# Kernel optimization log

Measured on AMD Instinct MI355X. Metric: run time of the kernel, lower is better.

## Reference

```python
import jax, jax.numpy as jnp
import numpy as np
from jax import lax

V, E, H = 32000, 512, 1024  # vocab, embedding_dim, hidden_dim
S, B, T = 50, 64, 10        # src len, batch, max decode steps
SOS = 0


def setup_inputs() -> dict:
    key = jax.random.key(0)
    ks = jax.random.split(key, 16)
    sc = 0.02
    n = jax.random.normal
    return {
        "enc_out": n(ks[0], (S, B, 2 * H), jnp.float32),
        "hidden": n(ks[1], (1, B, H), jnp.float32),
        "target": jax.random.randint(ks[2], (B, T), 0, V),
        "emb": n(ks[3], (V, E), jnp.float32) * sc,
        "w_ih": n(ks[4], (3 * H, E), jnp.float32) * sc,
        "w_hh": n(ks[5], (3 * H, H), jnp.float32) * sc,
        "b_ih": n(ks[6], (3 * H,), jnp.float32) * sc,
        "b_hh": n(ks[7], (3 * H,), jnp.float32) * sc,
        "wa_w": n(ks[8], (H, H), jnp.float32) * sc,
        "wa_b": n(ks[9], (H,), jnp.float32) * sc,
        "ua_w": n(ks[10], (H, 2 * H), jnp.float32) * sc,
        "ua_b": n(ks[11], (H,), jnp.float32) * sc,
        "va_w": n(ks[12], (1, H), jnp.float32) * sc,
        "va_b": n(ks[13], (1,), jnp.float32) * sc,
    }


def reference(enc_out, hidden, target, emb, w_ih, w_hh, b_ih, b_hh,
              wa_w, wa_b, ua_w, ua_b, va_w, va_b):
    b, t = target.shape

    def gru_cell(x, h):
        gi = x @ w_ih.T + b_ih          # [B, 3H]
        gh = h @ w_hh.T + b_hh          # [B, 3H]
        ir, iz, inn = jnp.split(gi, 3, axis=-1)
        hr, hz, hn = jnp.split(gh, 3, axis=-1)
        r = jax.nn.sigmoid(ir + hr)
        z = jax.nn.sigmoid(iz + hz)
        nng = jnp.tanh(inn + r * hn)
        return (1.0 - z) * nng + z * h

    # teacher-forced decoder inputs: [SOS, target[:, :-1]] -> [T, B]
    dec_in = jnp.concatenate(
        [jnp.full((b, 1), SOS, dtype=target.dtype), target[:, : t - 1]], axis=1)
    xs = emb[dec_in].transpose(1, 0, 2)  # [T, B, E] (dropout is identity in eval)

    def step(h, x):
        h2 = gru_cell(x, h)
        return h2, h2

    h_last, hs = lax.scan(step, hidden[0], xs)   # hs: [T, B, H]

    keys = enc_out.transpose(1, 0, 2)            # [B, S, 2H]
    uk = keys @ ua_w.T + ua_b                    # [B, S, H]
    wq = hs @ wa_w.T + wa_b                      # [T, B, H]
    # additive (Bahdanau) scores: [T, B, S]
    scores = (jnp.tanh(wq[:, :, None, :] + uk[None]) @ va_w.T + va_b)[..., 0]
    weights = jax.nn.softmax(scores, axis=-1)    # over source positions
    context = jnp.einsum('tbs,bsd->btd', weights, keys)  # [B, T, 2H]
    out = jax.nn.log_softmax(context, axis=-1)   # [B, T, 2H]
    return out, h_last
```

## Files before the change

kernel.cpp:

```cpp
#include <hip/hip_runtime.h>
#include <math.h>

#define VOCAB 32000
#define E_DIM 512
#define H_DIM 1024
#define S_LEN 50
#define B_SZ 64
#define T_LEN 10
#define H3 (3 * H_DIM)
#define D2H (2 * H_DIM)

typedef __attribute__((ext_vector_type(8))) short short8;
typedef __attribute__((ext_vector_type(4))) float floatx4;

__device__ __forceinline__ ushort f2b(float f) {
    union { float f; uint32_t u; } x; x.f = f;
    uint32_t r = (x.u + 0x7fff + ((x.u >> 16) & 1)) >> 16;
    return (ushort)r;
}
__device__ __forceinline__ float b2f(ushort u) {
    union { float f; uint32_t u; } x; x.u = ((uint32_t)u) << 16;
    return x.f;
}
__device__ __forceinline__ float fast_sigmoid(float x) {
    x = fminf(fmaxf(x, -30.f), 30.f);
    return 1.f / (1.f + __expf(-x));
}
__device__ __forceinline__ float fast_tanh(float x) {
    x = fminf(fmaxf(x, -15.f), 15.f);
    float e = __expf(2.f * x);
    return (e - 1.f) / (e + 1.f);
}

#define PB0 1536
#define PB1 (PB0 + 3072)
#define PB2 (PB1 + 2048)
#define PB3 (PB2 + 1024)
#define PB4 (PB3 + 3200)
#define PB5 (PB4 + 640)
#define PB6 (PB5 + 64)

__device__ __forceinline__ void cvt_chunk(const float* src, ushort* dst, int i) {
    float4 v = ((const float4*)src)[i];
    ushort4 o;
    o.x = f2b(v.x); o.y = f2b(v.y); o.z = f2b(v.z); o.w = f2b(v.w);
    ((ushort4*)dst)[i] = o;
}

__global__ __launch_bounds__(256) void prep(
    const float* __restrict__ w_ih, ushort* __restrict__ w_ihb,
    const float* __restrict__ w_hh, ushort* __restrict__ w_hhb,
    const float* __restrict__ ua_w, ushort* __restrict__ ua_wb,
    const float* __restrict__ wa_w, ushort* __restrict__ wa_wb,
    const float* __restrict__ enc_out, ushort* __restrict__ keysb,
    const int* __restrict__ target, const float* __restrict__ emb,
    ushort* __restrict__ Xb,
    const float* __restrict__ hidden, ushort* __restrict__ hb0,
    int* __restrict__ bar) {
    int bid = blockIdx.x, tid = threadIdx.x;
    if (bid == 0 && tid < 8) bar[tid] = 0;
    if (bid < PB0) {
        cvt_chunk(w_ih, w_ihb, bid * 256 + tid);
    } else if (bid < PB1) {
        cvt_chunk(w_hh, w_hhb, (bid - PB0) * 256 + tid);
    } else if (bid < PB2) {
        cvt_chunk(ua_w, ua_wb, (bid - PB1) * 256 + tid);
    } else if (bid < PB3) {
        cvt_chunk(wa_w, wa_wb, (bid - PB2) * 256 + tid);
    } else if (bid < PB4) {
        int bs = bid - PB3;
        int b = bs / S_LEN, s = bs % S_LEN;
        const float* src = enc_out + ((size_t)s * B_SZ + b) * D2H;
        ushort* dst = keysb + (size_t)bs * D2H;
#pragma unroll
        for (int p = 0; p < 2; ++p) {
            int i = tid + p * 256;
            float4 v = ((const float4*)src)[i];
            ushort4 o;
            o.x = f2b(v.x); o.y = f2b(v.y); o.z = f2b(v.z); o.w = f2b(v.w);
            ((ushort4*)dst)[i] = o;
        }
    } else if (bid < PB5) {
        int m = bid - PB4;
        int t = m / B_SZ, b = m % B_SZ;
        int idx = (t == 0) ? 0 : target[b * T_LEN + (t - 1)];
        if (tid < 128) {
            const float* src = emb + (size_t)idx * E_DIM;
            float4 v = ((const float4*)src)[tid];
            ushort4 o;
            o.x = f2b(v.x); o.y = f2b(v.y); o.z = f2b(v.z); o.w = f2b(v.w);
            ((ushort4*)(Xb + (size_t)m * E_DIM))[tid] = o;
        }
    } else {
        cvt_chunk(hidden, hb0, (bid - PB5) * 256 + tid);
    }
}

struct GemmArgs {
    const ushort* A; const ushort* W; const float* bias;
    float* Cf; ushort* C16;
    int M, N, K, nbn, nblk;
};

__global__ __launch_bounds__(256) void gemm_bf16(GemmArgs g0, GemmArgs g1) {
    const bool first = (int)blockIdx.x < g0.nblk;
    GemmArgs g = first ? g0 : g1;
    const int bid = first ? blockIdx.x : (blockIdx.x - g0.nblk);

    __shared__ ushort As[64 * 72];
    __shared__ ushort Bs[128 * 72];

    const int tid = threadIdx.x;
    const int w = tid >> 6, lane = tid & 63;
    const int lm = lane & 15, q = lane >> 4;
    const int wm = w >> 1, wn = w & 1;
    const int n0 = (bid % g.nbn) * 128;
    const int m0 = (bid / g.nbn) * 64;
    const int K = g.K;

    floatx4 acc[2][4];
#pragma unroll
    for (int i = 0; i < 2; ++i)
#pragma unroll
        for (int j = 0; j < 4; ++j)
            acc[i][j] = (floatx4){0.f, 0.f, 0.f, 0.f};

    short8 ar[2], br[4];
    auto load_tiles = [&](int k0) {
#pragma unroll
        for (int p = 0; p < 2; ++p) {
            int c = tid + p * 256;
            ar[p] = *(const short8*)&g.A[(size_t)(m0 + (c >> 3)) * K + k0 + (c & 7) * 8];
        }
#pragma unroll
        for (int p = 0; p < 4; ++p) {
            int c = tid + p * 256;
            br[p] = *(const short8*)&g.W[(size_t)(n0 + (c >> 3)) * K + k0 + (c & 7) * 8];
        }
    };

    load_tiles(0);
    for (int k0 = 0; k0 < K; k0 += 64) {
#pragma unroll
        for (int p = 0; p < 2; ++p) {
            int c = tid + p * 256;
            *(short8*)&As[(c >> 3) * 72 + (c & 7) * 8] = ar[p];
        }
#pragma unroll
        for (int p = 0; p < 4; ++p) {
            int c = tid + p * 256;
            *(short8*)&Bs[(c >> 3) * 72 + (c & 7) * 8] = br[p];
        }
        __syncthreads();
        if (k0 + 64 < K) load_tiles(k0 + 64);

#pragma unroll
        for (int kk = 0; kk < 2; ++kk) {
            short8 af[2], bf[4];
#pragma unroll
            for (int i = 0; i < 2; ++i)
                af[i] = *(const short8*)&As[(wm * 32 + i * 16 + lm) * 72 + kk * 32 + q * 8];
#pragma unroll
            for (int j = 0; j < 4; ++j)
                bf[j] = *(const short8*)&Bs[(wn * 64 + j * 16 + lm) * 72 + kk * 32 + q * 8];
#pragma unroll
            for (int i = 0; i < 2; ++i)
#pragma unroll
                for (int j = 0; j < 4; ++j)
                    acc[i][j] = __builtin_amdgcn_mfma_f32_16x16x32_bf16(af[i], bf[j], acc[i][j], 0, 0, 0);
        }
        __syncthreads();
    }

    float bv[4];
#pragma unroll
    for (int j = 0; j < 4; ++j)
        bv[j] = g.bias[n0 + wn * 64 + j * 16 + lm];
#pragma unroll
    for (int i = 0; i < 2; ++i) {
#pragma unroll
        for (int j = 0; j < 4; ++j) {
            int col = n0 + wn * 64 + j * 16 + lm;
#pragma unroll
            for (int r = 0; r < 4; ++r) {
                int row = m0 + wm * 32 + i * 16 + q * 4 + r;
                float v = acc[i][j][r] + bv[j];
                if (g.C16) g.C16[(size_t)row * g.N + col] = f2b(v);
                else       g.Cf[(size_t)row * g.N + col] = v;
            }
        }
    }
}

#define GRU_BLOCKS 64

__device__ __forceinline__ void grid_barrier(int* cnt, int* gen, int phase) {
    __syncthreads();
    if (threadIdx.x == 0) {
        __threadfence();
        if (atomicAdd(cnt, 1) == GRU_BLOCKS - 1) {
            atomicExch(cnt, 0);
            __threadfence();
            atomicExch(gen, phase + 1);
        } else {
            while (atomicAdd(gen, 0) <= phase) __builtin_amdgcn_s_sleep(8);
        }
        __threadfence();
    }
    __syncthreads();
}

__global__ __launch_bounds__(256) void gru_persistent(
    const ushort* __restrict__ w_hhb, const float* __restrict__ bhh,
    const float* __restrict__ GI, const float* __restrict__ hidden,
    ushort* __restrict__ hb0, ushort* __restrict__ hb1,
    ushort* __restrict__ hsb, float* __restrict__ outTail,
    int* __restrict__ bar) {
    __shared__ ushort Ws[2][48 * 136];
    const int tid = threadIdx.x;
    const int w = tid >> 6, lane = tid & 63;
    const int lm = lane & 15, q = lane >> 4;
    const int j0 = blockIdx.x * 16;
    const int j = j0 + lm;

    const float bhr = bhh[j], bhz = bhh[H_DIM + j], bhn = bhh[2 * H_DIM + j];

    float hf[4];
#pragma unroll
    for (int r = 0; r < 4; ++r)
        hf[r] = hidden[(size_t)(w * 16 + q * 4 + r) * H_DIM + j];

    short8 wr[3];
    auto stage_regs = [&](int kbase) {
#pragma unroll
        for (int p = 0; p < 3; ++p) {
            int c = tid + p * 256;
            int row = c >> 4, off = c & 15;
            int grow = (row >> 4) * H_DIM + j0 + (row & 15);
            wr[p] = *(const short8*)&w_hhb[(size_t)grow * H_DIM + kbase + off * 8];
        }
    };
    auto write_lds = [&](int buf) {
#pragma unroll
        for (int p = 0; p < 3; ++p) {
            int c = tid + p * 256;
            *(short8*)&Ws[buf][(c >> 4) * 136 + (c & 15) * 8] = wr[p];
        }
    };

    for (int t = 0; t < T_LEN; ++t) {
        const ushort* hin = (t & 1) ? hb1 : hb0;
        ushort* hout = (t & 1) ? hb0 : hb1;

        float ir[4], iz[4], inn[4];
#pragma unroll
        for (int r = 0; r < 4; ++r) {
            const float* gi = GI + (size_t)(t * B_SZ + w * 16 + q * 4 + r) * H3 + j;
            ir[r] = gi[0]; iz[r] = gi[H_DIM]; inn[r] = gi[2 * H_DIM];
        }

        floatx4 accr = {0.f, 0.f, 0.f, 0.f};
        floatx4 accz = {0.f, 0.f, 0.f, 0.f};
        floatx4 accn = {0.f, 0.f, 0.f, 0.f};

        stage_regs(0);
        write_lds(0);
        const ushort* arow = hin + (size_t)(w * 16 + lm) * H_DIM + q * 8;

        for (int it = 0; it < 8; ++it) {
            __syncthreads();
            if (it < 7) stage_regs((it + 1) * 128);
            short8 af[4];
#pragma unroll
            for (int kk = 0; kk < 4; ++kk)
                af[kk] = *(const short8*)&arow[it * 128 + kk * 32];
            const int buf = it & 1;
#pragma unroll
            for (int kk = 0; kk < 4; ++kk) {
                short8 b0 = *(const short8*)&Ws[buf][(lm) * 136 + kk * 32 + q * 8];
                short8 b1 = *(const short8*)&Ws[buf][(16 + lm) * 136 + kk * 32 + q * 8];
                short8 b2 = *(const short8*)&Ws[buf][(32 + lm) * 136 + kk * 32 + q * 8];
                accr = __builtin_amdgcn_mfma_f32_16x16x32_bf16(af[kk], b0, accr, 0, 0, 0);
                accz = __builtin_amdgcn_mfma_f32_16x16x32_bf16(af[kk], b1, accz, 0, 0, 0);
                accn = __builtin_amdgcn_mfma_f32_16x16x32_bf16(af[kk], b2, accn, 0, 0, 0);
            }
            if (it < 7) write_lds(buf ^ 1);
        }

#pragma unroll
        for (int r = 0; r < 4; ++r) {
            int b = w * 16 + q * 4 + r;
            float rg = fast_sigmoid(ir[r] + accr[r] + bhr);
            float z  = fast_sigmoid(iz[r] + accz[r] + bhz);
            float ng = fast_tanh(inn[r] + rg * (accn[r] + bhn));
            float hnew = (1.f - z) * ng + z * hf[r];
            hf[r] = hnew;
            size_t hi = (size_t)b * H_DIM + j;
            ushort h16 = f2b(hnew);
            hout[hi] = h16;
            hsb[(size_t)t * B_SZ * H_DIM + hi] = h16;
            if (t == T_LEN - 1) outTail[hi] = hnew;
        }

        if (t < T_LEN - 1) grid_barrier(&bar[0], &bar[1], t);
    }
}

__global__ __launch_bounds__(256) void attn_ctx(
    const ushort* __restrict__ WQ16, const ushort* __restrict__ UK16,
    const float* __restrict__ va_w, const float* __restrict__ va_b,
    const ushort* __restrict__ keysb, float* __restrict__ out) {
    __shared__ float wq_s[H_DIM];
    __shared__ float va_s[H_DIM];
    __shared__ float sc[S_LEN];
    __shared__ float wred[4];
    __shared__ float sred[4];
    const int bt = blockIdx.x;
    const int t = bt >> 6, b = bt & 63;
    const int tid = threadIdx.x;
    const int wave = tid >> 6, lane = tid & 63;

    for (int hh = tid; hh < H_DIM; hh += 256) {
        wq_s[hh] = b2f(WQ16[(size_t)(t * B_SZ + b) * H_DIM + hh]);
        va_s[hh] = va_w[hh];
    }
    __syncthreads();

    for (int s = wave; s < S_LEN; s += 4) {
        const ushort* uk = UK16 + ((size_t)b * S_LEN + s) * H_DIM + lane * 16;
        short8 u0 = *(const short8*)&uk[0];
        short8 u1 = *(const short8*)&uk[8];
        float acc = 0.f;
        const int h0 = lane * 16;
#pragma unroll
        for (int i = 0; i < 8; ++i)
            acc += fast_tanh(wq_s[h0 + i] + b2f((ushort)u0[i])) * va_s[h0 + i];
#pragma unroll
        for (int i = 0; i < 8; ++i)
            acc += fast_tanh(wq_s[h0 + 8 + i] + b2f((ushort)u1[i])) * va_s[h0 + 8 + i];
        for (int off = 32; off > 0; off >>= 1) acc += __shfl_down(acc, off);
        if (lane == 0) sc[s] = acc + va_b[0];
    }
    __syncthreads();

    if (tid < 64) {
        float v = (tid < S_LEN) ? sc[tid] : -INFINITY;
        float m = v;
        for (int off = 32; off > 0; off >>= 1) m = fmaxf(m, __shfl_down(m, off));
        m = __shfl(m, 0);
        float e = (tid < S_LEN) ? __expf(v - m) : 0.f;
        float sum = e;
        for (int off = 32; off > 0; off >>= 1) sum += __shfl_down(sum, off);
        sum = __shfl(sum, 0);
        if (tid < S_LEN) sc[tid] = e / sum;
    }
    __syncthreads();

    float c[8];
#pragma unroll
    for (int i = 0; i < 8; ++i) c[i] = 0.f;
    const ushort* kb = keysb + (size_t)b * S_LEN * D2H + tid * 8;
    for (int s = 0; s < S_LEN; ++s) {
        float ws = sc[s];
        short8 kv = *(const short8*)&kb[(size_t)s * D2H];
#pragma unroll
        for (int i = 0; i < 8; ++i) c[i] += ws * b2f((ushort)kv[i]);
    }

    float m = c[0];
#pragma unroll
    for (int i = 1; i < 8; ++i) m = fmaxf(m, c[i]);
    for (int off = 32; off > 0; off >>= 1) m = fmaxf(m, __shfl_down(m, off));
    if (lane == 0) wred[wave] = m;
    __syncthreads();
    if (tid == 0) wred[0] = fmaxf(fmaxf(wred[0], wred[1]), fmaxf(wred[2], wred[3]));
    __syncthreads();
    m = wred[0];
    float sum = 0.f;
#pragma unroll
    for (int i = 0; i < 8; ++i) sum += __expf(c[i] - m);
    for (int off = 32; off > 0; off >>= 1) sum += __shfl_down(sum, off);
    if (lane == 0) sred[wave] = sum;
    __syncthreads();
    if (tid == 0) sred[0] = sred[0] + sred[1] + sred[2] + sred[3];
    __syncthreads();
    float lse = m + __logf(sred[0]);

    float* o = out + ((size_t)b * T_LEN + t) * D2H + tid * 8;
#pragma unroll
    for (int i = 0; i < 8; ++i) o[i] = c[i] - lse;
}

extern "C" void kernel_launch(void* const* d_in, const int* in_sizes, int n_in,
                              void* d_out, int out_size, void* d_ws, size_t ws_size,
                              hipStream_t stream) {
    const float* enc_out = (const float*)d_in[0];
    const float* hidden  = (const float*)d_in[1];
    const int*   target  = (const int*)d_in[2];
    const float* emb     = (const float*)d_in[3];
    const float* w_ih    = (const float*)d_in[4];
    const float* w_hh    = (const float*)d_in[5];
    const float* b_ih    = (const float*)d_in[6];
    const float* b_hh    = (const float*)d_in[7];
    const float* wa_w    = (const float*)d_in[8];
    const float* wa_b    = (const float*)d_in[9];
    const float* ua_w    = (const float*)d_in[10];
    const float* ua_b    = (const float*)d_in[11];
    const float* va_w    = (const float*)d_in[12];
    const float* va_b    = (const float*)d_in[13];
    float* out = (float*)d_out;

    const int TB = T_LEN * B_SZ;
    const int BS = B_SZ * S_LEN;

    char* p = (char*)d_ws;
    int*    bar   = (int*)p;    p += 256;
    float*  GI    = (float*)p;  p += (size_t)TB * H3 * 4;
    p = (char*)(((uintptr_t)p + 255) & ~(uintptr_t)255);
    ushort* keysb = (ushort*)p; p += (size_t)BS * D2H * 2;
    ushort* Xb    = (ushort*)p; p += (size_t)TB * E_DIM * 2;
    ushort* w_ihb = (ushort*)p; p += (size_t)H3 * E_DIM * 2;
    ushort* w_hhb = (ushort*)p; p += (size_t)H3 * H_DIM * 2;
    ushort* ua_wb = (ushort*)p; p += (size_t)H_DIM * D2H * 2;
    ushort* wa_wb = (ushort*)p; p += (size_t)H_DIM * H_DIM * 2;
    ushort* hb0   = (ushort*)p; p += (size_t)B_SZ * H_DIM * 2;
    ushort* hb1   = (ushort*)p; p += (size_t)B_SZ * H_DIM * 2;
    ushort* hsb   = (ushort*)p; p += (size_t)TB * H_DIM * 2;
    ushort* UK16  = (ushort*)p; p += (size_t)BS * H_DIM * 2;
    ushort* WQ16  = (ushort*)p; p += (size_t)TB * H_DIM * 2;

    prep<<<PB6, 256, 0, stream>>>(w_ih, w_ihb, w_hh, w_hhb, ua_w, ua_wb, wa_w, wa_wb,
                                  enc_out, keysb, target, emb, Xb, hidden, hb0, bar);

    GemmArgs guk = { keysb, ua_wb, ua_b, nullptr, UK16,
                     BS, H_DIM, D2H, H_DIM / 128, (BS / 64) * (H_DIM / 128) };
    GemmArgs ggi = { Xb, w_ihb, b_ih, GI, nullptr,
                     TB, H3, E_DIM, H3 / 128, (TB / 64) * (H3 / 128) };
    gemm_bf16<<<guk.nblk + ggi.nblk, 256, 0, stream>>>(guk, ggi);

    float* outTail = out + (size_t)B_SZ * T_LEN * D2H;
    gru_persistent<<<GRU_BLOCKS, 256, 0, stream>>>(w_hhb, b_hh, GI, hidden,
                                                   hb0, hb1, hsb, outTail, bar);

    GemmArgs gwq = { hsb, wa_wb, wa_b, nullptr, WQ16,
                     TB, H_DIM, H_DIM, H_DIM / 128, (TB / 64) * (H_DIM / 128) };
    gemm_bf16<<<gwq.nblk, 256, 0, stream>>>(gwq, gwq);

    attn_ctx<<<B_SZ * T_LEN, 256, 0, stream>>>(WQ16, UK16, va_w, va_b, keysb, out);
}
```

Before: 355.8 us.

## Keep GRU recurrent weight slice resident in LDS and use hierarchical grid barrier

The persistent GRU kernel now loads each block's 48x1024 bf16 slice of w_hh into LDS once, before the time loop, instead of re-streaming it from global memory every step through double-buffered tiles. This removes per-step weight traffic and the per-tile __syncthreads, and the hidden-state A fragments are prefetched one tile ahead. The grid barrier becomes a two-level counter tree with per-step slots (8 groups of 8 blocks, padded to separate lines), using acquire/release atomics and a shorter sleep, to cut contention on a single atomic. The cost is about 99 KB of LDS per block and a larger barrier workspace that prep now zeroes.

```diff
diff --git a/kernel.cpp b/kernel.cpp
--- a/kernel.cpp
+++ b/kernel.cpp
@@ -58,7 +58,9 @@
     const float* __restrict__ hidden, ushort* __restrict__ hb0,
     int* __restrict__ bar) {
     int bid = blockIdx.x, tid = threadIdx.x;
-    if (bid == 0 && tid < 8) bar[tid] = 0;
+    if (bid == 0) {
+        for (int i = tid; i < 4096; i += 256) bar[i] = 0;
+    }
     if (bid < PB0) {
         cvt_chunk(w_ih, w_ihb, bid * 256 + tid);
     } else if (bid < PB1) {
@@ -193,18 +195,25 @@
 }
 
 #define GRU_BLOCKS 64
-
-__device__ __forceinline__ void grid_barrier(int* cnt, int* gen, int phase) {
+#define WS_STRIDE 1032
+
+__device__ __forceinline__ void grid_barrier(int* __restrict__ bar, int t, int bid) {
     __syncthreads();
     if (threadIdx.x == 0) {
         __threadfence();
-        if (atomicAdd(cnt, 1) == GRU_BLOCKS - 1) {
-            atomicExch(cnt, 0);
-            __threadfence();
-            atomicExch(gen, phase + 1);
-        } else {
-            while (atomicAdd(gen, 0) <= phase) __builtin_amdgcn_s_sleep(8);
-        }
+        int g = bid & 7;
+        int sub = __hip_atomic_fetch_add(&bar[(t * 8 + g) * 32], 1,
+                                         __ATOMIC_ACQ_REL, __HIP_MEMORY_SCOPE_AGENT);
+        if (sub == 7) {
+            int m = __hip_atomic_fetch_add(&bar[2560 + t * 32], 1,
+                                           __ATOMIC_ACQ_REL, __HIP_MEMORY_SCOPE_AGENT);
+            if (m == 7)
+                __hip_atomic_store(&bar[3040], t + 1,
+                                   __ATOMIC_RELEASE, __HIP_MEMORY_SCOPE_AGENT);
+        }
+        while (__hip_atomic_load(&bar[3040], __ATOMIC_ACQUIRE,
+                                 __HIP_MEMORY_SCOPE_AGENT) <= t)
+            __builtin_amdgcn_s_sleep(2);
         __threadfence();
     }
     __syncthreads();
@@ -216,12 +225,22 @@
     ushort* __restrict__ hb0, ushort* __restrict__ hb1,
     ushort* __restrict__ hsb, float* __restrict__ outTail,
     int* __restrict__ bar) {
-    __shared__ ushort Ws[2][48 * 136];
+    __shared__ ushort Ws[48 * WS_STRIDE];
     const int tid = threadIdx.x;
     const int w = tid >> 6, lane = tid & 63;
     const int lm = lane & 15, q = lane >> 4;
-    const int j0 = blockIdx.x * 16;
+    const int bid = blockIdx.x;
+    const int j0 = bid * 16;
     const int j = j0 + lm;
+
+#pragma unroll
+    for (int p = 0; p < 24; ++p) {
+        int c = tid + p * 256;
+        int row = c >> 7, off = c & 127;
+        int grow = (row >> 4) * H_DIM + j0 + (row & 15);
+        *(short8*)&Ws[row * WS_STRIDE + off * 8] =
+            *(const short8*)&w_hhb[(size_t)grow * H_DIM + off * 8];
+    }
 
     const float bhr = bhh[j], bhz = bhh[H_DIM + j], bhn = bhh[2 * H_DIM + j];
 
@@ -230,23 +249,7 @@
     for (int r = 0; r < 4; ++r)
         hf[r] = hidden[(size_t)(w * 16 + q * 4 + r) * H_DIM + j];
 
-    short8 wr[3];
-    auto stage_regs = [&](int kbase) {
-#pragma unroll
-        for (int p = 0; p < 3; ++p) {
-            int c = tid + p * 256;
-            int row = c >> 4, off = c & 15;
-            int grow = (row >> 4) * H_DIM + j0 + (row & 15);
-            wr[p] = *(const short8*)&w_hhb[(size_t)grow * H_DIM + kbase + off * 8];
-        }
-    };
-    auto write_lds = [&](int buf) {
-#pragma unroll
-        for (int p = 0; p < 3; ++p) {
-            int c = tid + p * 256;
-            *(short8*)&Ws[buf][(c >> 4) * 136 + (c & 15) * 8] = wr[p];
-        }
-    };
+    __syncthreads();
 
     for (int t = 0; t < T_LEN; ++t) {
         const ushort* hin = (t & 1) ? hb1 : hb0;
@@ -263,28 +266,32 @@
         floatx4 accz = {0.f, 0.f, 0.f, 0.f};
         floatx4 accn = {0.f, 0.f, 0.f, 0.f};
 
-        stage_regs(0);
-        write_lds(0);
         const ushort* arow = hin + (size_t)(w * 16 + lm) * H_DIM + q * 8;
 
+        short8 af[4], afn[4];
+#pragma unroll
+        for (int kk = 0; kk < 4; ++kk)
+            afn[kk] = *(const short8*)&arow[kk * 32];
+
+#pragma unroll
         for (int it = 0; it < 8; ++it) {
-            __syncthreads();
-            if (it < 7) stage_regs((it + 1) * 128);
-            short8 af[4];
-#pragma unroll
-            for (int kk = 0; kk < 4; ++kk)
-                af[kk] = *(const short8*)&arow[it * 128 + kk * 32];
-            const int buf = it & 1;
+#pragma unroll
+            for (int kk = 0; kk < 4; ++kk) af[kk] = afn[kk];
+            if (it < 7) {
+#pragma unroll
+                for (int kk = 0; kk < 4; ++kk)
+                    afn[kk] = *(const short8*)&arow[(it + 1) * 128 + kk * 32];
+            }
 #pragma unroll
             for (int kk = 0; kk < 4; ++kk) {
-                short8 b0 = *(const short8*)&Ws[buf][(lm) * 136 + kk * 32 + q * 8];
-                short8 b1 = *(const short8*)&Ws[buf][(16 + lm) * 136 + kk * 32 + q * 8];
-                short8 b2 = *(const short8*)&Ws[buf][(32 + lm) * 136 + kk * 32 + q * 8];
+                const int ko = it * 128 + kk * 32 + q * 8;
+                short8 b0 = *(const short8*)&Ws[(lm) * WS_STRIDE + ko];
+                short8 b1 = *(const short8*)&Ws[(16 + lm) * WS_STRIDE + ko];
+                short8 b2 = *(const short8*)&Ws[(32 + lm) * WS_STRIDE + ko];
                 accr = __builtin_amdgcn_mfma_f32_16x16x32_bf16(af[kk], b0, accr, 0, 0, 0);
                 accz = __builtin_amdgcn_mfma_f32_16x16x32_bf16(af[kk], b1, accz, 0, 0, 0);
                 accn = __builtin_amdgcn_mfma_f32_16x16x32_bf16(af[kk], b2, accn, 0, 0, 0);
             }
-            if (it < 7) write_lds(buf ^ 1);
         }
 
 #pragma unroll
@@ -302,7 +309,7 @@
             if (t == T_LEN - 1) outTail[hi] = hnew;
         }
 
-        if (t < T_LEN - 1) grid_barrier(&bar[0], &bar[1], t);
+        if (t < T_LEN - 1) grid_barrier(bar, t, bid);
     }
 }
 
@@ -414,7 +421,7 @@
     const int BS = B_SZ * S_LEN;
 
     char* p = (char*)d_ws;
-    int*    bar   = (int*)p;    p += 256;
+    int*    bar   = (int*)p;    p += 4096 * 4;
     float*  GI    = (float*)p;  p += (size_t)TB * H3 * 4;
     p = (char*)(((uintptr_t)p + 255) & ~(uintptr_t)255);
     ushort* keysb = (ushort*)p; p += (size_t)BS * D2H * 2;
```

Result: faster. 348.1 us (-2.2%).
